# Kernel tuning notes

Measured on AMD Instinct MI355X. Metric: run time of the kernel, lower is better.

Reference implementation:

```python
import jax, jax.numpy as jnp
import numpy as np

B, S, D, E, H, K = 4, 2048, 1024, 8, 4096, 2


def setup_inputs() -> dict:
    key = jax.random.key(0)
    ks = jax.random.split(key, 6)
    scale_in = 0.02  # keep logits/activations in a sane range
    return {
        "x": jax.random.normal(ks[0], (B, S, D), jnp.float32),
        "gate_w": jax.random.normal(ks[1], (D, E), jnp.float32) * scale_in,
        "noise_weight": jnp.zeros((E,), jnp.float32),  # torch init: zeros
        "noise": jax.random.normal(ks[2], (B, S, E), jnp.float32),
        "w1": jax.random.normal(ks[3], (E, D, H), jnp.float32) * scale_in,
        "b1": jnp.zeros((E, H), jnp.float32),
        "w2": jax.random.normal(ks[4], (E, D, H), jnp.float32) * scale_in,
        "b2": jnp.zeros((E, H), jnp.float32),
        "wp": jax.random.normal(ks[5], (E, H, D), jnp.float32) * scale_in,
        "bp": jnp.zeros((E, D), jnp.float32),
    }


def _moe(x, gate_w, noise_weight, noise, w1, b1, w2, b2, wp, bp):
    b, s, d = x.shape
    # --- noisy top-k gate ---
    logits = jnp.einsum("bsd,de->bse", x, gate_w)          # [B,S,E]
    logits_noisy = logits + noise * noise_weight            # noisy_std = 1.0
    top_v, top_i = jax.lax.top_k(logits_noisy, K)           # [B,S,K]
    # softmax over sparse logits (-inf elsewhere) == softmax over the top-k values
    probs_k = jax.nn.softmax(top_v, axis=-1)                # [B,S,K]
    onehot = jax.nn.one_hot(top_i, E, dtype=x.dtype)        # [B,S,K,E]
    gated = jnp.einsum("bsk,bske->bse", probs_k, onehot)    # [B,S,E]

    # --- dispatch / expert SwiGLU / weighted combine ---
    xf = x.reshape(b * s, d)                                # [T,D]
    gf = gated.reshape(b * s, E).T                          # [E,T]

    def body(acc, p):
        w1e, b1e, w2e, b2e, wpe, bpe, ge = p
        h = (xf @ w1e + b1e) * jax.nn.silu(xf @ w2e + b2e)  # [T,H] SwiGLU
        out = h @ wpe + bpe                                 # [T,D]
        return acc + ge[:, None] * out, None

    acc, _ = jax.lax.scan(body, jnp.zeros_like(xf), (w1, b1, w2, b2, wp, bp, gf))
    return acc.reshape(b, s, d)


def reference(x, gate_w, noise_weight, noise, w1, b1, w2, b2, wp, bp):
    return _moe(x, gate_w, noise_weight, noise, w1, b1, w2, b2, wp, bp)
```

## Files before the change

### kernel.cpp

```cpp
#include <hip/hip_runtime.h>


#define T_TOK 8192
#define DDIM 1024
#define EEXP 8
#define HDIM 4096
#define RMAX 18432

typedef short short8 __attribute__((ext_vector_type(8)));
typedef float f32x4 __attribute__((ext_vector_type(4)));
typedef unsigned short ushort4v __attribute__((ext_vector_type(4)));
typedef unsigned int u32;

__device__ __forceinline__ unsigned short f2bf(float f) {
  unsigned u = __builtin_bit_cast(unsigned, f);
  return (unsigned short)((u + 0x7FFFu + ((u >> 16) & 1u)) >> 16);
}
__device__ __forceinline__ float bf2f(unsigned short b) {
  unsigned u = ((unsigned)b) << 16;
  return __builtin_bit_cast(float, u);
}
__device__ __forceinline__ void gl_lds16(const void* g, void* l) {
  __builtin_amdgcn_global_load_lds((const u32 __attribute__((address_space(1)))*)g,
                                   (u32 __attribute__((address_space(3)))*)l, 16, 0, 0);
}
#define BAR() asm volatile("s_barrier" ::: "memory")
__device__ __forceinline__ void vwait_c(int n) {
  if (n == 8) asm volatile("s_waitcnt vmcnt(8)" ::: "memory");
  else if (n == 4) asm volatile("s_waitcnt vmcnt(4)" ::: "memory");
  else if (n == 0) asm volatile("s_waitcnt vmcnt(0)" ::: "memory");
}
#define MFMA_BF16 __builtin_amdgcn_mfma_f32_16x16x32_bf16

__device__ __forceinline__ int swz(int r, int kc16) {
  return (r * 64) ^ kc16 ^ (((r >> 1) & 7) << 4);
}

__global__ void k_convert_all(const float* __restrict__ w1, const float* __restrict__ w2,
                              const float* __restrict__ wp,
                              unsigned short* __restrict__ w1s, unsigned short* __restrict__ w2s,
                              unsigned short* __restrict__ wps) {
  __shared__ float lbuf[32][130];
  int bid = blockIdx.x;
  int seg = bid >> 13;
  int t = bid & 8191;
  const float* src; unsigned short* dst; int N, K, ct, kt, e;
  e = t >> 10;
  if (seg < 2) {
    src = (seg == 0) ? w1 : w2; dst = (seg == 0) ? w1s : w2s;
    N = HDIM; K = DDIM; ct = (t >> 5) & 31; kt = t & 31;
  } else {
    src = wp; dst = wps;
    N = DDIM; K = HDIM; ct = (t >> 7) & 7; kt = t & 127;
  }
  int tid = threadIdx.x;
  const float* s = src + (size_t)e * K * N + (size_t)(kt * 32) * N + ct * 128;
#pragma unroll
  for (int q = 0; q < 4; q++) {
    int idx = q * 256 + tid;
    int row = idx >> 5, c4 = (idx & 31) * 4;
    float4 v = *(const float4*)(s + (size_t)row * N + c4);
    lbuf[row][c4 + 0] = v.x; lbuf[row][c4 + 1] = v.y;
    lbuf[row][c4 + 2] = v.z; lbuf[row][c4 + 3] = v.w;
  }
  __syncthreads();
  char* dt = (char*)dst + ((size_t)(e * (N / 128) + ct) * (K / 32) + kt) * 8192;
#pragma unroll
  for (int q = 0; q < 2; q++) {
    int idx = q * 256 + tid;
    int n = idx >> 2, kc = idx & 3;
    short8 o;
#pragma unroll
    for (int j = 0; j < 8; j++) o[j] = (short)f2bf(lbuf[kc * 8 + j][n]);
    *(short8*)(dt + swz(n, kc * 16)) = o;
  }
}

__global__ void k_init(int* __restrict__ rowtok, int* __restrict__ counts, int* __restrict__ cursor) {
  int i = blockIdx.x * 256 + threadIdx.x;
  if (i < RMAX) rowtok[i] = 0;
  if (i < EEXP) { counts[i] = 0; cursor[i] = 0; }
}

__launch_bounds__(256)
__global__ void k_gate(const float* __restrict__ x, const float* __restrict__ gw,
                       const float* __restrict__ nwt, const float* __restrict__ noi,
                       int* __restrict__ tki, float* __restrict__ tkp,
                       int* __restrict__ counts, unsigned short* __restrict__ xb) {
  __shared__ float gwT[8][1024];
  int tid = threadIdx.x;
#pragma unroll
  for (int q = 0; q < 32; q++) {
    int flat = q * 256 + tid;
    gwT[flat & 7][flat >> 3] = gw[flat];
  }
  __syncthreads();
  int wave = tid >> 6, l = tid & 63;
  int t = blockIdx.x * 4 + wave;
  float acc[8] = {0.f, 0.f, 0.f, 0.f, 0.f, 0.f, 0.f, 0.f};
  const float4* xr = (const float4*)(x + (size_t)t * DDIM);
#pragma unroll
  for (int i = 0; i < 4; i++) {
    float4 xv = xr[l + i * 64];
    int d0 = (l + i * 64) * 4;
    ushort4v o;
    o.x = f2bf(xv.x); o.y = f2bf(xv.y); o.z = f2bf(xv.z); o.w = f2bf(xv.w);
    *(ushort4v*)(xb + (size_t)t * DDIM + d0) = o;
#pragma unroll
    for (int e = 0; e < 8; e++) {
      float4 gv = *(const float4*)&gwT[e][d0];
      acc[e] += xv.x * gv.x + xv.y * gv.y + xv.z * gv.z + xv.w * gv.w;
    }
  }
#pragma unroll
  for (int s = 1; s < 64; s <<= 1) {
#pragma unroll
    for (int e = 0; e < 8; e++) acc[e] += __shfl_xor(acc[e], s, 64);
  }
  if (l == 0) {
    float nl[8];
#pragma unroll
    for (int e = 0; e < 8; e++) nl[e] = acc[e] + noi[t * 8 + e] * nwt[e];
    int i0 = 0; float v0 = nl[0];
#pragma unroll
    for (int e = 1; e < 8; e++) if (nl[e] > v0) { v0 = nl[e]; i0 = e; }
    int i1 = -1; float v1 = -3.4e38f;
#pragma unroll
    for (int e = 0; e < 8; e++) if (e != i0 && nl[e] > v1) { v1 = nl[e]; i1 = e; }
    float ex = __expf(v1 - v0);
    float p0 = 1.f / (1.f + ex);
    float p1 = ex * p0;
    tki[2 * t] = i0; tki[2 * t + 1] = i1;
    tkp[2 * t] = p0; tkp[2 * t + 1] = p1;
    atomicAdd(&counts[i0], 1);
    atomicAdd(&counts[i1], 1);
  }
}

__global__ void k_prefix(const int* __restrict__ counts, int* __restrict__ basep) {
  if (threadIdx.x == 0) {
    int b = 0;
    for (int e = 0; e < EEXP; e++) { basep[e] = b; b += (counts[e] + 255) & ~255; }
  }
}

__global__ void k_scatter(const int* __restrict__ tki, const int* __restrict__ basep,
                          int* __restrict__ cursor, int* __restrict__ rowtok,
                          int* __restrict__ t2r) {
  int t = blockIdx.x * 256 + threadIdx.x;
  if (t >= T_TOK) return;
#pragma unroll
  for (int k = 0; k < 2; k++) {
    int e = tki[2 * t + k];
    int pos = atomicAdd(&cursor[e], 1);
    int row = basep[e] + pos;
    rowtok[row] = t;
    t2r[2 * t + k] = row;
  }
}

#define INV_MAP(c, r, kc) { int _h = (c) >> 3;                                   \
    r = 2 * _h + ((((c) >> 2) ^ (_h >> 2)) & 1);                                 \
    kc = ((c) & 3) ^ (_h & 3); }

__launch_bounds__(512, 2)
__global__ void k_gemm1(const unsigned short* __restrict__ xb,
                        const unsigned short* __restrict__ w1s, const unsigned short* __restrict__ w2s,
                        const float* __restrict__ b1g, const float* __restrict__ b2g,
                        const int* __restrict__ counts, const int* __restrict__ basep,
                        const int* __restrict__ rowtok,
                        unsigned short* __restrict__ hout) {
  int e = blockIdx.y >> 6;
  int rt = blockIdx.y & 63;
  int cnt = counts[e];
  if (rt >= ((cnt + 255) >> 8)) return;
  int ct = blockIdx.x;
  int row0 = basep[e] + rt * 256;
  int col0 = ct * 128;

  __shared__ char smem[131072];
  __shared__ int s_tok[256];
  __shared__ float s_b1[128], s_b2[128];

  int tid = threadIdx.x;
  if (tid < 256) s_tok[tid] = rowtok[row0 + tid];
  if (tid < 128) {
    s_b1[tid] = b1g[e * HDIM + col0 + tid];
    s_b2[tid] = b2g[e * HDIM + col0 + tid];
  }
  __syncthreads();

  int wave = tid >> 6, l = tid & 63;
  int wm = wave >> 2, wn = wave & 3;
  int g = l >> 4, ln = l & 15;

  int c0 = tid, c1 = 512 + tid;
  int r0, kc0, r1, kc1;
  INV_MAP(c0, r0, kc0) INV_MAP(c1, r1, kc1)
  size_t a_src0 = (size_t)s_tok[r0] * 2048 + (size_t)(kc0 * 16);
  size_t a_src1 = (size_t)s_tok[r1] * 2048 + (size_t)(kc1 * 16);
  int a_dst0 = c0 * 16, a_dst1 = c1 * 16;

  int a_rd[8];
#pragma unroll
  for (int m = 0; m < 8; m++) {
    int r = wm * 128 + m * 16 + ln;
    a_rd[m] = swz(r, g * 16);
  }
  int b_rd[2];
#pragma unroll
  for (int n = 0; n < 2; n++) {
    int r = wn * 32 + n * 16 + ln;
    b_rd[n] = swz(r, g * 16);
  }

  f32x4 zero = {0.f, 0.f, 0.f, 0.f};
  f32x4 acc_a[8][2], acc_b[8][2];
#pragma unroll
  for (int m = 0; m < 8; m++)
#pragma unroll
    for (int n = 0; n < 2; n++) { acc_a[m][n] = zero; acc_b[m][n] = zero; }

  const char* xbb = (const char*)xb;
  const char* w1t = (const char*)w1s + (size_t)(e * 32 + ct) * 32 * 8192;
  const char* w2t = (const char*)w2s + (size_t)(e * 32 + ct) * 32 * 8192;

#define G1_PRE(s) { int nb = (s) & 3;                                            \
    gl_lds16(xbb + a_src0 + (size_t)(s) * 64, smem + nb * 16384 + a_dst0);       \
    gl_lds16(xbb + a_src1 + (size_t)(s) * 64, smem + nb * 16384 + a_dst1);       \
    gl_lds16(w1t + (size_t)(s) * 8192 + tid * 16, smem + 65536 + nb * 8192 + tid * 16); \
    gl_lds16(w2t + (size_t)(s) * 8192 + tid * 16, smem + 98304 + nb * 8192 + tid * 16); }

  G1_PRE(0) G1_PRE(1) G1_PRE(2)
  vwait_c(8); BAR();

#define G1_SLOT(s, ISSUE, VMN) {                                                 \
    int bs = (s) & 3;                                                            \
    char* Ab = smem + bs * 16384;                                                \
    char* B1b = smem + 65536 + bs * 8192;                                        \
    char* B2b = smem + 98304 + bs * 8192;                                        \
    short8 af[4], b1f[2], b2f[2];                                                \
    _Pragma("unroll") for (int m = 0; m < 4; m++) af[m] = *(const short8*)(Ab + a_rd[m]); \
    b1f[0] = *(const short8*)(B1b + b_rd[0]); b1f[1] = *(const short8*)(B1b + b_rd[1]); \
    b2f[0] = *(const short8*)(B2b + b_rd[0]); b2f[1] = *(const short8*)(B2b + b_rd[1]); \
    if (ISSUE) { int ns = (s) + 3, nb = ns & 3;                                  \
      gl_lds16(xbb + a_src0 + (size_t)ns * 64, smem + nb * 16384 + a_dst0);      \
      gl_lds16(xbb + a_src1 + (size_t)ns * 64, smem + nb * 16384 + a_dst1); }    \
    BAR();                                                                       \
    __builtin_amdgcn_s_setprio(1);                                               \
    _Pragma("unroll") for (int m = 0; m < 4; m++) {                              \
      acc_a[m][0] = MFMA_BF16(af[m], b1f[0], acc_a[m][0], 0, 0, 0);              \
      acc_a[m][1] = MFMA_BF16(af[m], b1f[1], acc_a[m][1], 0, 0, 0);              \
      acc_b[m][0] = MFMA_BF16(af[m], b2f[0], acc_b[m][0], 0, 0, 0);              \
      acc_b[m][1] = MFMA_BF16(af[m], b2f[1], acc_b[m][1], 0, 0, 0); }            \
    __builtin_amdgcn_s_setprio(0);                                               \
    BAR();                                                                       \
    _Pragma("unroll") for (int m = 0; m < 4; m++) af[m] = *(const short8*)(Ab + a_rd[4 + m]); \
    if (ISSUE) { int ns = (s) + 3, nb = ns & 3;                                  \
      gl_lds16(w1t + (size_t)ns * 8192 + tid * 16, smem + 65536 + nb * 8192 + tid * 16); \
      gl_lds16(w2t + (size_t)ns * 8192 + tid * 16, smem + 98304 + nb * 8192 + tid * 16); } \
    BAR();                                                                       \
    __builtin_amdgcn_s_setprio(1);                                               \
    _Pragma("unroll") for (int m = 0; m < 4; m++) {                              \
      acc_a[4 + m][0] = MFMA_BF16(af[m], b1f[0], acc_a[4 + m][0], 0, 0, 0);      \
      acc_a[4 + m][1] = MFMA_BF16(af[m], b1f[1], acc_a[4 + m][1], 0, 0, 0);      \
      acc_b[4 + m][0] = MFMA_BF16(af[m], b2f[0], acc_b[4 + m][0], 0, 0, 0);      \
      acc_b[4 + m][1] = MFMA_BF16(af[m], b2f[1], acc_b[4 + m][1], 0, 0, 0); }    \
    __builtin_amdgcn_s_setprio(0);                                               \
    vwait_c(VMN); BAR(); }

  for (int s = 0; s < 29; ++s) { G1_SLOT(s, 1, 8) }
  G1_SLOT(29, 0, 4)
  G1_SLOT(30, 0, 0)
  G1_SLOT(31, 0, -1)

  __syncthreads();
  unsigned short* ht = (unsigned short*)smem;
#pragma unroll
  for (int m = 0; m < 8; m++)
#pragma unroll
    for (int n = 0; n < 2; n++)
#pragma unroll
      for (int r = 0; r < 4; r++) {
        int row = wm * 128 + m * 16 + g * 4 + r;
        int col = wn * 32 + n * 16 + ln;
        float a = acc_a[m][n][r] + s_b1[col];
        float b = acc_b[m][n][r] + s_b2[col];
        float hv = a * (b / (1.f + __expf(-b)));
        ht[row * 128 + col] = f2bf(hv);
      }
  __syncthreads();
#pragma unroll
  for (int q = 0; q < 8; q++) {
    int idx = q * 512 + tid;
    int row = idx >> 4, cc = (idx & 15) * 8;
    short8 v = *(const short8*)(smem + idx * 16);
    *(short8*)(hout + (size_t)(row0 + row) * HDIM + col0 + cc) = v;
  }
}

__launch_bounds__(512, 2)
__global__ void k_gemm2(const unsigned short* __restrict__ hin,
                        const unsigned short* __restrict__ wps, const float* __restrict__ bpg,
                        const int* __restrict__ counts, const int* __restrict__ basep,
                        unsigned short* __restrict__ yout) {
  int e = blockIdx.y >> 6;
  int rt = blockIdx.y & 63;
  int cnt = counts[e];
  if (rt >= ((cnt + 255) >> 8)) return;
  int ct = blockIdx.x;
  int row0 = basep[e] + rt * 256;
  int col0 = ct * 256;

  __shared__ char smem[131072];
  __shared__ float s_bp[256];
  int tid = threadIdx.x;
  if (tid < 256) s_bp[tid] = bpg[e * DDIM + col0 + tid];
  __syncthreads();

  int wave = tid >> 6, l = tid & 63;
  int wm = wave >> 2, wn = wave & 3;
  int g = l >> 4, ln = l & 15;

  int c0 = tid, c1 = 512 + tid;
  int r0, kc0, r1, kc1;
  INV_MAP(c0, r0, kc0) INV_MAP(c1, r1, kc1)
  size_t a_src0 = (size_t)(row0 + r0) * 8192 + (size_t)(kc0 * 16);
  size_t a_src1 = (size_t)(row0 + r1) * 8192 + (size_t)(kc1 * 16);
  int a_dst0 = c0 * 16, a_dst1 = c1 * 16;
  const char* b_src0 = (const char*)wps + (size_t)(e * 8 + ct * 2 + 0) * 128 * 8192 + (size_t)tid * 16;
  const char* b_src1 = (const char*)wps + (size_t)(e * 8 + ct * 2 + 1) * 128 * 8192 + (size_t)tid * 16;

  int a_rd[8];
#pragma unroll
  for (int m = 0; m < 8; m++) {
    int r = wm * 128 + m * 16 + ln;
    a_rd[m] = swz(r, g * 16);
  }
  int b_rd[4];
#pragma unroll
  for (int n = 0; n < 4; n++) {
    int ncol = wn * 64 + n * 16 + ln;
    int sub = ncol >> 7, r = ncol & 127;
    b_rd[n] = sub * 8192 + swz(r, g * 16);
  }

  f32x4 zero = {0.f, 0.f, 0.f, 0.f};
  f32x4 acc[8][4];
#pragma unroll
  for (int m = 0; m < 8; m++)
#pragma unroll
    for (int n = 0; n < 4; n++) acc[m][n] = zero;

  const char* hb = (const char*)hin;

#define G2_PRE(s) { int nb = (s) & 3;                                            \
    gl_lds16(hb + a_src0 + (size_t)(s) * 64, smem + nb * 16384 + a_dst0);        \
    gl_lds16(hb + a_src1 + (size_t)(s) * 64, smem + nb * 16384 + a_dst1);        \
    gl_lds16(b_src0 + (size_t)(s) * 8192, smem + 65536 + nb * 16384 + tid * 16); \
    gl_lds16(b_src1 + (size_t)(s) * 8192, smem + 65536 + nb * 16384 + 8192 + tid * 16); }

  G2_PRE(0) G2_PRE(1) G2_PRE(2)
  vwait_c(8); BAR();

#define G2_SLOT(s, ISSUE, VMN) {                                                 \
    int bs = (s) & 3;                                                            \
    char* Ab = smem + bs * 16384;                                                \
    char* Bb = smem + 65536 + bs * 16384;                                        \
    short8 af[4], bf[4];                                                         \
    _Pragma("unroll") for (int m = 0; m < 4; m++) af[m] = *(const short8*)(Ab + a_rd[m]); \
    _Pragma("unroll") for (int n = 0; n < 4; n++) bf[n] = *(const short8*)(Bb + b_rd[n]); \
    if (ISSUE) { int ns = (s) + 3, nb = ns & 3;                                  \
      gl_lds16(hb + a_src0 + (size_t)ns * 64, smem + nb * 16384 + a_dst0);       \
      gl_lds16(hb + a_src1 + (size_t)ns * 64, smem + nb * 16384 + a_dst1); }     \
    BAR();                                                                       \
    __builtin_amdgcn_s_setprio(1);                                               \
    _Pragma("unroll") for (int m = 0; m < 4; m++)                                \
      _Pragma("unroll") for (int n = 0; n < 4; n++)                              \
        acc[m][n] = MFMA_BF16(af[m], bf[n], acc[m][n], 0, 0, 0);                 \
    __builtin_amdgcn_s_setprio(0);                                               \
    BAR();                                                                       \
    _Pragma("unroll") for (int m = 0; m < 4; m++) af[m] = *(const short8*)(Ab + a_rd[4 + m]); \
    if (ISSUE) { int ns = (s) + 3, nb = ns & 3;                                  \
      gl_lds16(b_src0 + (size_t)ns * 8192, smem + 65536 + nb * 16384 + tid * 16);\
      gl_lds16(b_src1 + (size_t)ns * 8192, smem + 65536 + nb * 16384 + 8192 + tid * 16); }\
    BAR();                                                                       \
    __builtin_amdgcn_s_setprio(1);                                               \
    _Pragma("unroll") for (int m = 0; m < 4; m++)                                \
      _Pragma("unroll") for (int n = 0; n < 4; n++)                              \
        acc[4 + m][n] = MFMA_BF16(af[m], bf[n], acc[4 + m][n], 0, 0, 0);         \
    __builtin_amdgcn_s_setprio(0);                                               \
    vwait_c(VMN); BAR(); }

  for (int s = 0; s < 125; ++s) { G2_SLOT(s, 1, 8) }
  G2_SLOT(125, 0, 4)
  G2_SLOT(126, 0, 0)
  G2_SLOT(127, 0, -1)

  __syncthreads();
  unsigned short* ht = (unsigned short*)smem;
#pragma unroll
  for (int m = 0; m < 8; m++)
#pragma unroll
    for (int n = 0; n < 4; n++)
#pragma unroll
      for (int r = 0; r < 4; r++) {
        int row = wm * 128 + m * 16 + g * 4 + r;
        int col = wn * 64 + n * 16 + ln;
        ht[row * 256 + col] = f2bf(acc[m][n][r] + s_bp[col]);
      }
  __syncthreads();
#pragma unroll
  for (int q = 0; q < 16; q++) {
    int idx = q * 512 + tid;
    int row = idx >> 5, cc = (idx & 31) * 8;
    short8 v = *(const short8*)(smem + idx * 16);
    *(short8*)(yout + (size_t)(row0 + row) * DDIM + col0 + cc) = v;
  }
}

__global__ void k_combine(const unsigned short* __restrict__ yv,
                          const int* __restrict__ t2r, const float* __restrict__ tkp,
                          float* __restrict__ outp) {
  int gid = blockIdx.x * 256 + threadIdx.x;
  int t = gid >> 8;
  int c4 = (gid & 255) << 2;
  int r0 = t2r[2 * t], r1 = t2r[2 * t + 1];
  float p0 = tkp[2 * t], p1 = tkp[2 * t + 1];
  ushort4v u0 = *(const ushort4v*)(yv + (size_t)r0 * DDIM + c4);
  ushort4v u1 = *(const ushort4v*)(yv + (size_t)r1 * DDIM + c4);
  float4 o;
  o.x = p0 * bf2f(u0.x) + p1 * bf2f(u1.x);
  o.y = p0 * bf2f(u0.y) + p1 * bf2f(u1.y);
  o.z = p0 * bf2f(u0.z) + p1 * bf2f(u1.z);
  o.w = p0 * bf2f(u0.w) + p1 * bf2f(u1.w);
  *(float4*)(outp + (size_t)t * DDIM + c4) = o;
}

extern "C" void kernel_launch(void* const* d_in, const int* in_sizes, int n_in,
                              void* d_out, int out_size, void* d_ws, size_t ws_size,
                              hipStream_t stream) {
  const float* x   = (const float*)d_in[0];
  const float* gw  = (const float*)d_in[1];
  const float* nwt = (const float*)d_in[2];
  const float* noi = (const float*)d_in[3];
  const float* w1  = (const float*)d_in[4];
  const float* b1  = (const float*)d_in[5];
  const float* w2  = (const float*)d_in[6];
  const float* b2  = (const float*)d_in[7];
  const float* wp  = (const float*)d_in[8];
  const float* bp  = (const float*)d_in[9];
  float* outp = (float*)d_out;
  char* ws = (char*)d_ws;

  constexpr size_t SZ_W = (size_t)EEXP * DDIM * HDIM * 2;
  constexpr size_t OFF_XB  = 0;
  constexpr size_t OFF_W1S = OFF_XB + (size_t)T_TOK * DDIM * 2;
  constexpr size_t OFF_W2S = OFF_W1S + SZ_W;
  constexpr size_t OFF_WPS = OFF_W2S + SZ_W;
  constexpr size_t OFF_H   = OFF_WPS + SZ_W;
  constexpr size_t OFF_Y   = OFF_H + (size_t)RMAX * HDIM * 2;
  constexpr size_t OFF_RT  = OFF_Y + (size_t)RMAX * DDIM * 2;
  constexpr size_t OFF_TKI = OFF_RT + (size_t)RMAX * 4;
  constexpr size_t OFF_TKP = OFF_TKI + (size_t)T_TOK * 2 * 4;
  constexpr size_t OFF_T2R = OFF_TKP + (size_t)T_TOK * 2 * 4;
  constexpr size_t OFF_CNT = OFF_T2R + (size_t)T_TOK * 2 * 4;
  constexpr size_t OFF_BAS = OFF_CNT + 256;
  constexpr size_t OFF_CUR = OFF_BAS + 256;

  unsigned short* xb  = (unsigned short*)(ws + OFF_XB);
  unsigned short* w1s = (unsigned short*)(ws + OFF_W1S);
  unsigned short* w2s = (unsigned short*)(ws + OFF_W2S);
  unsigned short* wps = (unsigned short*)(ws + OFF_WPS);
  unsigned short* h   = (unsigned short*)(ws + OFF_H);
  unsigned short* y   = (unsigned short*)(ws + OFF_Y);
  int*   rowtok = (int*)(ws + OFF_RT);
  int*   tki    = (int*)(ws + OFF_TKI);
  float* tkp    = (float*)(ws + OFF_TKP);
  int*   t2r    = (int*)(ws + OFF_T2R);
  int*   counts = (int*)(ws + OFF_CNT);
  int*   basep  = (int*)(ws + OFF_BAS);
  int*   cursor = (int*)(ws + OFF_CUR);

  dim3 blk(256);
  k_init<<<dim3((RMAX + 255) / 256), blk, 0, stream>>>(rowtok, counts, cursor);
  k_gate<<<dim3(T_TOK / 4), blk, 0, stream>>>(x, gw, nwt, noi, tki, tkp, counts, xb);
  k_convert_all<<<dim3(24576), blk, 0, stream>>>(w1, w2, wp, w1s, w2s, wps);
  k_prefix<<<dim3(1), dim3(64), 0, stream>>>(counts, basep);
  k_scatter<<<dim3(T_TOK / 256), blk, 0, stream>>>(tki, basep, cursor, rowtok, t2r);
  k_gemm1<<<dim3(HDIM / 128, EEXP * 64), dim3(512), 0, stream>>>(xb, w1s, w2s, b1, b2, counts, basep, rowtok, h);
  k_gemm2<<<dim3(DDIM / 256, EEXP * 64), dim3(512), 0, stream>>>(h, wps, bp, counts, basep, y);
  k_combine<<<dim3(T_TOK), blk, 0, stream>>>(y, t2r, tkp, outp);
  (void)in_sizes; (void)n_in; (void)out_size; (void)ws_size;
}
```

Measured before the change: 1.029 ms.

## Switch expert GEMMs to 3-stage LDS ring with prefetch depth two

Both expert GEMM kernels move from a 4-buffer, prefetch-distance-3 LDS pipeline to a 3-buffer ring with prefetch distance 2. The wait-then-barrier now sits at the top of each k-step, and each stage stores A and B interleaved in one 32KB slot. LDS per block drops from 128KB to 96KB, and launch bounds are relaxed to one block per CU, presumably to free registers and shorten the pipeline. The GEMM2 epilogue now stages its output in two halves so it fits the smaller LDS, at the cost of an extra barrier pair and less latency hiding for global loads.

```diff
diff --git a/kernel.cpp b/kernel.cpp
--- a/kernel.cpp
+++ b/kernel.cpp
@@ -25,16 +25,16 @@
                                    (u32 __attribute__((address_space(3)))*)l, 16, 0, 0);
 }
 #define BAR() asm volatile("s_barrier" ::: "memory")
-__device__ __forceinline__ void vwait_c(int n) {
-  if (n == 8) asm volatile("s_waitcnt vmcnt(8)" ::: "memory");
-  else if (n == 4) asm volatile("s_waitcnt vmcnt(4)" ::: "memory");
-  else if (n == 0) asm volatile("s_waitcnt vmcnt(0)" ::: "memory");
-}
+#define VW4() asm volatile("s_waitcnt vmcnt(4)" ::: "memory")
+#define VW0() asm volatile("s_waitcnt vmcnt(0)" ::: "memory")
 #define MFMA_BF16 __builtin_amdgcn_mfma_f32_16x16x32_bf16
 
 __device__ __forceinline__ int swz(int r, int kc16) {
   return (r * 64) ^ kc16 ^ (((r >> 1) & 7) << 4);
 }
+#define INV_MAP(c, r, kc) { int _h = (c) >> 3;                                   \
+    r = 2 * _h + ((((c) >> 2) ^ (_h >> 2)) & 1);                                 \
+    kc = ((c) & 3) ^ (_h & 3); }
 
 __global__ void k_convert_all(const float* __restrict__ w1, const float* __restrict__ w2,
                               const float* __restrict__ wp,
@@ -159,11 +159,7 @@
   }
 }
 
-#define INV_MAP(c, r, kc) { int _h = (c) >> 3;                                   \
-    r = 2 * _h + ((((c) >> 2) ^ (_h >> 2)) & 1);                                 \
-    kc = ((c) & 3) ^ (_h & 3); }
-
-__launch_bounds__(512, 2)
+__launch_bounds__(512, 1)
 __global__ void k_gemm1(const unsigned short* __restrict__ xb,
                         const unsigned short* __restrict__ w1s, const unsigned short* __restrict__ w2s,
                         const float* __restrict__ b1g, const float* __restrict__ b2g,
@@ -178,7 +174,7 @@
   int row0 = basep[e] + rt * 256;
   int col0 = ct * 128;
 
-  __shared__ char smem[131072];
+  __shared__ char smem[98304];
   __shared__ int s_tok[256];
   __shared__ float s_b1[128], s_b2[128];
 
@@ -225,54 +221,86 @@
   const char* w1t = (const char*)w1s + (size_t)(e * 32 + ct) * 32 * 8192;
   const char* w2t = (const char*)w2s + (size_t)(e * 32 + ct) * 32 * 8192;
 
-#define G1_PRE(s) { int nb = (s) & 3;                                            \
-    gl_lds16(xbb + a_src0 + (size_t)(s) * 64, smem + nb * 16384 + a_dst0);       \
-    gl_lds16(xbb + a_src1 + (size_t)(s) * 64, smem + nb * 16384 + a_dst1);       \
-    gl_lds16(w1t + (size_t)(s) * 8192 + tid * 16, smem + 65536 + nb * 8192 + tid * 16); \
-    gl_lds16(w2t + (size_t)(s) * 8192 + tid * 16, smem + 98304 + nb * 8192 + tid * 16); }
-
-  G1_PRE(0) G1_PRE(1) G1_PRE(2)
-  vwait_c(8); BAR();
-
-#define G1_SLOT(s, ISSUE, VMN) {                                                 \
-    int bs = (s) & 3;                                                            \
-    char* Ab = smem + bs * 16384;                                                \
-    char* B1b = smem + 65536 + bs * 8192;                                        \
-    char* B2b = smem + 98304 + bs * 8192;                                        \
-    short8 af[4], b1f[2], b2f[2];                                                \
-    _Pragma("unroll") for (int m = 0; m < 4; m++) af[m] = *(const short8*)(Ab + a_rd[m]); \
-    b1f[0] = *(const short8*)(B1b + b_rd[0]); b1f[1] = *(const short8*)(B1b + b_rd[1]); \
-    b2f[0] = *(const short8*)(B2b + b_rd[0]); b2f[1] = *(const short8*)(B2b + b_rd[1]); \
-    if (ISSUE) { int ns = (s) + 3, nb = ns & 3;                                  \
-      gl_lds16(xbb + a_src0 + (size_t)ns * 64, smem + nb * 16384 + a_dst0);      \
-      gl_lds16(xbb + a_src1 + (size_t)ns * 64, smem + nb * 16384 + a_dst1); }    \
-    BAR();                                                                       \
-    __builtin_amdgcn_s_setprio(1);                                               \
-    _Pragma("unroll") for (int m = 0; m < 4; m++) {                              \
-      acc_a[m][0] = MFMA_BF16(af[m], b1f[0], acc_a[m][0], 0, 0, 0);              \
-      acc_a[m][1] = MFMA_BF16(af[m], b1f[1], acc_a[m][1], 0, 0, 0);              \
-      acc_b[m][0] = MFMA_BF16(af[m], b2f[0], acc_b[m][0], 0, 0, 0);              \
-      acc_b[m][1] = MFMA_BF16(af[m], b2f[1], acc_b[m][1], 0, 0, 0); }            \
-    __builtin_amdgcn_s_setprio(0);                                               \
-    BAR();                                                                       \
-    _Pragma("unroll") for (int m = 0; m < 4; m++) af[m] = *(const short8*)(Ab + a_rd[4 + m]); \
-    if (ISSUE) { int ns = (s) + 3, nb = ns & 3;                                  \
-      gl_lds16(w1t + (size_t)ns * 8192 + tid * 16, smem + 65536 + nb * 8192 + tid * 16); \
-      gl_lds16(w2t + (size_t)ns * 8192 + tid * 16, smem + 98304 + nb * 8192 + tid * 16); } \
-    BAR();                                                                       \
-    __builtin_amdgcn_s_setprio(1);                                               \
-    _Pragma("unroll") for (int m = 0; m < 4; m++) {                              \
-      acc_a[4 + m][0] = MFMA_BF16(af[m], b1f[0], acc_a[4 + m][0], 0, 0, 0);      \
-      acc_a[4 + m][1] = MFMA_BF16(af[m], b1f[1], acc_a[4 + m][1], 0, 0, 0);      \
-      acc_b[4 + m][0] = MFMA_BF16(af[m], b2f[0], acc_b[4 + m][0], 0, 0, 0);      \
-      acc_b[4 + m][1] = MFMA_BF16(af[m], b2f[1], acc_b[4 + m][1], 0, 0, 0); }    \
-    __builtin_amdgcn_s_setprio(0);                                               \
-    vwait_c(VMN); BAR(); }
-
-  for (int s = 0; s < 29; ++s) { G1_SLOT(s, 1, 8) }
-  G1_SLOT(29, 0, 4)
-  G1_SLOT(30, 0, 0)
-  G1_SLOT(31, 0, -1)
+#pragma unroll
+  for (int s = 0; s < 2; s++) {
+    char* nb = smem + s * 32768;
+    gl_lds16(xbb + a_src0 + (size_t)s * 64, nb + a_dst0);
+    gl_lds16(w1t + (size_t)s * 8192 + tid * 16, nb + 16384 + tid * 16);
+    gl_lds16(xbb + a_src1 + (size_t)s * 64, nb + a_dst1);
+    gl_lds16(w2t + (size_t)s * 8192 + tid * 16, nb + 24576 + tid * 16);
+  }
+
+  const int NT = 32;
+  int bc = 0;
+  for (int s = 0; s < NT; ++s) {
+    if (s < NT - 1) VW4(); else VW0();
+    BAR();
+    char* buf = smem + bc * 32768;
+    int nbi = bc + 2; if (nbi >= 3) nbi -= 3;
+    char* nbuf = smem + nbi * 32768;
+    bool pf = (s < NT - 2);
+    short8 af0, af1, af2, af3, b1f0, b1f1, b2f0, b2f1;
+    af0 = *(const short8*)(buf + a_rd[0]);
+    af1 = *(const short8*)(buf + a_rd[1]);
+    af2 = *(const short8*)(buf + a_rd[2]);
+    af3 = *(const short8*)(buf + a_rd[3]);
+    b1f0 = *(const short8*)(buf + 16384 + b_rd[0]);
+    b1f1 = *(const short8*)(buf + 16384 + b_rd[1]);
+    b2f0 = *(const short8*)(buf + 24576 + b_rd[0]);
+    b2f1 = *(const short8*)(buf + 24576 + b_rd[1]);
+    if (pf) {
+      gl_lds16(xbb + a_src0 + (size_t)(s + 2) * 64, nbuf + a_dst0);
+      gl_lds16(w1t + (size_t)(s + 2) * 8192 + tid * 16, nbuf + 16384 + tid * 16);
+    }
+    BAR();
+    __builtin_amdgcn_s_setprio(1);
+    acc_a[0][0] = MFMA_BF16(af0, b1f0, acc_a[0][0], 0, 0, 0);
+    acc_a[0][1] = MFMA_BF16(af0, b1f1, acc_a[0][1], 0, 0, 0);
+    acc_b[0][0] = MFMA_BF16(af0, b2f0, acc_b[0][0], 0, 0, 0);
+    acc_b[0][1] = MFMA_BF16(af0, b2f1, acc_b[0][1], 0, 0, 0);
+    acc_a[1][0] = MFMA_BF16(af1, b1f0, acc_a[1][0], 0, 0, 0);
+    acc_a[1][1] = MFMA_BF16(af1, b1f1, acc_a[1][1], 0, 0, 0);
+    acc_b[1][0] = MFMA_BF16(af1, b2f0, acc_b[1][0], 0, 0, 0);
+    acc_b[1][1] = MFMA_BF16(af1, b2f1, acc_b[1][1], 0, 0, 0);
+    acc_a[2][0] = MFMA_BF16(af2, b1f0, acc_a[2][0], 0, 0, 0);
+    acc_a[2][1] = MFMA_BF16(af2, b1f1, acc_a[2][1], 0, 0, 0);
+    acc_b[2][0] = MFMA_BF16(af2, b2f0, acc_b[2][0], 0, 0, 0);
+    acc_b[2][1] = MFMA_BF16(af2, b2f1, acc_b[2][1], 0, 0, 0);
+    acc_a[3][0] = MFMA_BF16(af3, b1f0, acc_a[3][0], 0, 0, 0);
+    acc_a[3][1] = MFMA_BF16(af3, b1f1, acc_a[3][1], 0, 0, 0);
+    acc_b[3][0] = MFMA_BF16(af3, b2f0, acc_b[3][0], 0, 0, 0);
+    acc_b[3][1] = MFMA_BF16(af3, b2f1, acc_b[3][1], 0, 0, 0);
+    __builtin_amdgcn_s_setprio(0);
+    BAR();
+    af0 = *(const short8*)(buf + a_rd[4]);
+    af1 = *(const short8*)(buf + a_rd[5]);
+    af2 = *(const short8*)(buf + a_rd[6]);
+    af3 = *(const short8*)(buf + a_rd[7]);
+    if (pf) {
+      gl_lds16(xbb + a_src1 + (size_t)(s + 2) * 64, nbuf + a_dst1);
+      gl_lds16(w2t + (size_t)(s + 2) * 8192 + tid * 16, nbuf + 24576 + tid * 16);
+    }
+    BAR();
+    __builtin_amdgcn_s_setprio(1);
+    acc_a[4][0] = MFMA_BF16(af0, b1f0, acc_a[4][0], 0, 0, 0);
+    acc_a[4][1] = MFMA_BF16(af0, b1f1, acc_a[4][1], 0, 0, 0);
+    acc_b[4][0] = MFMA_BF16(af0, b2f0, acc_b[4][0], 0, 0, 0);
+    acc_b[4][1] = MFMA_BF16(af0, b2f1, acc_b[4][1], 0, 0, 0);
+    acc_a[5][0] = MFMA_BF16(af1, b1f0, acc_a[5][0], 0, 0, 0);
+    acc_a[5][1] = MFMA_BF16(af1, b1f1, acc_a[5][1], 0, 0, 0);
+    acc_b[5][0] = MFMA_BF16(af1, b2f0, acc_b[5][0], 0, 0, 0);
+    acc_b[5][1] = MFMA_BF16(af1, b2f1, acc_b[5][1], 0, 0, 0);
+    acc_a[6][0] = MFMA_BF16(af2, b1f0, acc_a[6][0], 0, 0, 0);
+    acc_a[6][1] = MFMA_BF16(af2, b1f1, acc_a[6][1], 0, 0, 0);
+    acc_b[6][0] = MFMA_BF16(af2, b2f0, acc_b[6][0], 0, 0, 0);
+    acc_b[6][1] = MFMA_BF16(af2, b2f1, acc_b[6][1], 0, 0, 0);
+    acc_a[7][0] = MFMA_BF16(af3, b1f0, acc_a[7][0], 0, 0, 0);
+    acc_a[7][1] = MFMA_BF16(af3, b1f1, acc_a[7][1], 0, 0, 0);
+    acc_b[7][0] = MFMA_BF16(af3, b2f0, acc_b[7][0], 0, 0, 0);
+    acc_b[7][1] = MFMA_BF16(af3, b2f1, acc_b[7][1], 0, 0, 0);
+    __builtin_amdgcn_s_setprio(0);
+    bc++; if (bc == 3) bc = 0;
+  }
 
   __syncthreads();
   unsigned short* ht = (unsigned short*)smem;
@@ -299,7 +327,7 @@
   }
 }
 
-__launch_bounds__(512, 2)
+__launch_bounds__(512, 1)
 __global__ void k_gemm2(const unsigned short* __restrict__ hin,
                         const unsigned short* __restrict__ wps, const float* __restrict__ bpg,
                         const int* __restrict__ counts, const int* __restrict__ basep,
@@ -312,7 +340,7 @@
   int row0 = basep[e] + rt * 256;
   int col0 = ct * 256;
 
-  __shared__ char smem[131072];
+  __shared__ char smem[98304];
   __shared__ float s_bp[256];
   int tid = threadIdx.x;
   if (tid < 256) s_bp[tid] = bpg[e * DDIM + col0 + tid];
@@ -342,7 +370,7 @@
   for (int n = 0; n < 4; n++) {
     int ncol = wn * 64 + n * 16 + ln;
     int sub = ncol >> 7, r = ncol & 127;
-    b_rd[n] = sub * 8192 + swz(r, g * 16);
+    b_rd[n] = 16384 + sub * 8192 + swz(r, g * 16);
   }
 
   f32x4 zero = {0.f, 0.f, 0.f, 0.f};
@@ -354,68 +382,111 @@
 
   const char* hb = (const char*)hin;
 
-#define G2_PRE(s) { int nb = (s) & 3;                                            \
-    gl_lds16(hb + a_src0 + (size_t)(s) * 64, smem + nb * 16384 + a_dst0);        \
-    gl_lds16(hb + a_src1 + (size_t)(s) * 64, smem + nb * 16384 + a_dst1);        \
-    gl_lds16(b_src0 + (size_t)(s) * 8192, smem + 65536 + nb * 16384 + tid * 16); \
-    gl_lds16(b_src1 + (size_t)(s) * 8192, smem + 65536 + nb * 16384 + 8192 + tid * 16); }
-
-  G2_PRE(0) G2_PRE(1) G2_PRE(2)
-  vwait_c(8); BAR();
-
-#define G2_SLOT(s, ISSUE, VMN) {                                                 \
-    int bs = (s) & 3;                                                            \
-    char* Ab = smem + bs * 16384;                                                \
-    char* Bb = smem + 65536 + bs * 16384;                                        \
-    short8 af[4], bf[4];                                                         \
-    _Pragma("unroll") for (int m = 0; m < 4; m++) af[m] = *(const short8*)(Ab + a_rd[m]); \
-    _Pragma("unroll") for (int n = 0; n < 4; n++) bf[n] = *(const short8*)(Bb + b_rd[n]); \
-    if (ISSUE) { int ns = (s) + 3, nb = ns & 3;                                  \
-      gl_lds16(hb + a_src0 + (size_t)ns * 64, smem + nb * 16384 + a_dst0);       \
-      gl_lds16(hb + a_src1 + (size_t)ns * 64, smem + nb * 16384 + a_dst1); }     \
-    BAR();                                                                       \
-    __builtin_amdgcn_s_setprio(1);                                               \
-    _Pragma("unroll") for (int m = 0; m < 4; m++)                                \
-      _Pragma("unroll") for (int n = 0; n < 4; n++)                              \
-        acc[m][n] = MFMA_BF16(af[m], bf[n], acc[m][n], 0, 0, 0);                 \
-    __builtin_amdgcn_s_setprio(0);                                               \
-    BAR();                                                                       \
-    _Pragma("unroll") for (int m = 0; m < 4; m++) af[m] = *(const short8*)(Ab + a_rd[4 + m]); \
-    if (ISSUE) { int ns = (s) + 3, nb = ns & 3;                                  \
-      gl_lds16(b_src0 + (size_t)ns * 8192, smem + 65536 + nb * 16384 + tid * 16);\
-      gl_lds16(b_src1 + (size_t)ns * 8192, smem + 65536 + nb * 16384 + 8192 + tid * 16); }\
-    BAR();                                                                       \
-    __builtin_amdgcn_s_setprio(1);                                               \
-    _Pragma("unroll") for (int m = 0; m < 4; m++)                                \
-      _Pragma("unroll") for (int n = 0; n < 4; n++)                              \
-        acc[4 + m][n] = MFMA_BF16(af[m], bf[n], acc[4 + m][n], 0, 0, 0);         \
-    __builtin_amdgcn_s_setprio(0);                                               \
-    vwait_c(VMN); BAR(); }
-
-  for (int s = 0; s < 125; ++s) { G2_SLOT(s, 1, 8) }
-  G2_SLOT(125, 0, 4)
-  G2_SLOT(126, 0, 0)
-  G2_SLOT(127, 0, -1)
-
-  __syncthreads();
+#pragma unroll
+  for (int s = 0; s < 2; s++) {
+    char* nb = smem + s * 32768;
+    gl_lds16(hb + a_src0 + (size_t)s * 64, nb + a_dst0);
+    gl_lds16(b_src0 + (size_t)s * 8192, nb + 16384 + tid * 16);
+    gl_lds16(hb + a_src1 + (size_t)s * 64, nb + a_dst1);
+    gl_lds16(b_src1 + (size_t)s * 8192, nb + 24576 + tid * 16);
+  }
+
+  const int NT = 128;
+  int bc = 0;
+  for (int s = 0; s < NT; ++s) {
+    if (s < NT - 1) VW4(); else VW0();
+    BAR();
+    char* buf = smem + bc * 32768;
+    int nbi = bc + 2; if (nbi >= 3) nbi -= 3;
+    char* nbuf = smem + nbi * 32768;
+    bool pf = (s < NT - 2);
+    short8 af0, af1, af2, af3, bf0, bf1, bf2, bf3;
+    af0 = *(const short8*)(buf + a_rd[0]);
+    af1 = *(const short8*)(buf + a_rd[1]);
+    af2 = *(const short8*)(buf + a_rd[2]);
+    af3 = *(const short8*)(buf + a_rd[3]);
+    bf0 = *(const short8*)(buf + b_rd[0]);
+    bf1 = *(const short8*)(buf + b_rd[1]);
+    bf2 = *(const short8*)(buf + b_rd[2]);
+    bf3 = *(const short8*)(buf + b_rd[3]);
+    if (pf) {
+      gl_lds16(hb + a_src0 + (size_t)(s + 2) * 64, nbuf + a_dst0);
+      gl_lds16(b_src0 + (size_t)(s + 2) * 8192, nbuf + 16384 + tid * 16);
+    }
+    BAR();
+    __builtin_amdgcn_s_setprio(1);
+    acc[0][0] = MFMA_BF16(af0, bf0, acc[0][0], 0, 0, 0);
+    acc[0][1] = MFMA_BF16(af0, bf1, acc[0][1], 0, 0, 0);
+    acc[0][2] = MFMA_BF16(af0, bf2, acc[0][2], 0, 0, 0);
+    acc[0][3] = MFMA_BF16(af0, bf3, acc[0][3], 0, 0, 0);
+    acc[1][0] = MFMA_BF16(af1, bf0, acc[1][0], 0, 0, 0);
+    acc[1][1] = MFMA_BF16(af1, bf1, acc[1][1], 0, 0, 0);
+    acc[1][2] = MFMA_BF16(af1, bf2, acc[1][2], 0, 0, 0);
+    acc[1][3] = MFMA_BF16(af1, bf3, acc[1][3], 0, 0, 0);
+    acc[2][0] = MFMA_BF16(af2, bf0, acc[2][0], 0, 0, 0);
+    acc[2][1] = MFMA_BF16(af2, bf1, acc[2][1], 0, 0, 0);
+    acc[2][2] = MFMA_BF16(af2, bf2, acc[2][2], 0, 0, 0);
+    acc[2][3] = MFMA_BF16(af2, bf3, acc[2][3], 0, 0, 0);
+    acc[3][0] = MFMA_BF16(af3, bf0, acc[3][0], 0, 0, 0);
+    acc[3][1] = MFMA_BF16(af3, bf1, acc[3][1], 0, 0, 0);
+    acc[3][2] = MFMA_BF16(af3, bf2, acc[3][2], 0, 0, 0);
+    acc[3][3] = MFMA_BF16(af3, bf3, acc[3][3], 0, 0, 0);
+    __builtin_amdgcn_s_setprio(0);
+    BAR();
+    af0 = *(const short8*)(buf + a_rd[4]);
+    af1 = *(const short8*)(buf + a_rd[5]);
+    af2 = *(const short8*)(buf + a_rd[6]);
+    af3 = *(const short8*)(buf + a_rd[7]);
+    if (pf) {
+      gl_lds16(hb + a_src1 + (size_t)(s + 2) * 64, nbuf + a_dst1);
+      gl_lds16(b_src1 + (size_t)(s + 2) * 8192, nbuf + 24576 + tid * 16);
+    }
+    BAR();
+    __builtin_amdgcn_s_setprio(1);
+    acc[4][0] = MFMA_BF16(af0, bf0, acc[4][0], 0, 0, 0);
+    acc[4][1] = MFMA_BF16(af0, bf1, acc[4][1], 0, 0, 0);
+    acc[4][2] = MFMA_BF16(af0, bf2, acc[4][2], 0, 0, 0);
+    acc[4][3] = MFMA_BF16(af0, bf3, acc[4][3], 0, 0, 0);
+    acc[5][0] = MFMA_BF16(af1, bf0, acc[5][0], 0, 0, 0);
+    acc[5][1] = MFMA_BF16(af1, bf1, acc[5][1], 0, 0, 0);
+    acc[5][2] = MFMA_BF16(af1, bf2, acc[5][2], 0, 0, 0);
+    acc[5][3] = MFMA_BF16(af1, bf3, acc[5][3], 0, 0, 0);
+    acc[6][0] = MFMA_BF16(af2, bf0, acc[6][0], 0, 0, 0);
+    acc[6][1] = MFMA_BF16(af2, bf1, acc[6][1], 0, 0, 0);
+    acc[6][2] = MFMA_BF16(af2, bf2, acc[6][2], 0, 0, 0);
+    acc[6][3] = MFMA_BF16(af2, bf3, acc[6][3], 0, 0, 0);
+    acc[7][0] = MFMA_BF16(af3, bf0, acc[7][0], 0, 0, 0);
+    acc[7][1] = MFMA_BF16(af3, bf1, acc[7][1], 0, 0, 0);
+    acc[7][2] = MFMA_BF16(af3, bf2, acc[7][2], 0, 0, 0);
+    acc[7][3] = MFMA_BF16(af3, bf3, acc[7][3], 0, 0, 0);
+    __builtin_amdgcn_s_setprio(0);
+    bc++; if (bc == 3) bc = 0;
+  }
+
   unsigned short* ht = (unsigned short*)smem;
 #pragma unroll
-  for (int m = 0; m < 8; m++)
-#pragma unroll
-    for (int n = 0; n < 4; n++)
-#pragma unroll
-      for (int r = 0; r < 4; r++) {
-        int row = wm * 128 + m * 16 + g * 4 + r;
-        int col = wn * 64 + n * 16 + ln;
-        ht[row * 256 + col] = f2bf(acc[m][n][r] + s_bp[col]);
-      }
-  __syncthreads();
-#pragma unroll
-  for (int q = 0; q < 16; q++) {
-    int idx = q * 512 + tid;
-    int row = idx >> 5, cc = (idx & 31) * 8;
-    short8 v = *(const short8*)(smem + idx * 16);
-    *(short8*)(yout + (size_t)(row0 + row) * DDIM + col0 + cc) = v;
+  for (int p = 0; p < 2; p++) {
+    __syncthreads();
+    if ((wn >> 1) == p) {
+#pragma unroll
+      for (int m = 0; m < 8; m++)
+#pragma unroll
+        for (int n = 0; n < 4; n++)
+#pragma unroll
+          for (int r = 0; r < 4; r++) {
+            int row = wm * 128 + m * 16 + g * 4 + r;
+            int col = wn * 64 + n * 16 + ln;
+            ht[row * 128 + (col - p * 128)] = f2bf(acc[m][n][r] + s_bp[col]);
+          }
+    }
+    __syncthreads();
+#pragma unroll
+    for (int q = 0; q < 8; q++) {
+      int idx = q * 512 + tid;
+      int row = idx >> 4, cc = (idx & 15) * 8;
+      short8 v = *(const short8*)(smem + idx * 16);
+      *(short8*)(yout + (size_t)(row0 + row) * DDIM + col0 + p * 128 + cc) = v;
+    }
   }
 }
 
```

Measured after the change: 1.054 ms. 2.4% more time.
